# Optimization experiments

Measured on AMD Instinct MI355X. Metric: run time of the kernel, lower is better.

Reference implementation:

```python
import jax, jax.numpy as jnp
import numpy as np

L = 7
LVL = 3
B = 8
R = 16
N = 4 ** L  # 16384
P = N // 4  # number of local blocks
T = 4 * R   # ConvLocal output features


def build_permutation_indices(L, l):
    delta = 4 ** (L - l - 1)
    tmp = np.tile(np.arange(4) * delta, delta)
    tmp += np.repeat(np.arange(delta), 4)
    tmp = np.tile(tmp, 4 ** l)
    tmp += np.repeat(np.arange(4 ** l) * 4 ** (L - l), 4 ** (L - l))
    return jnp.asarray(tmp, dtype=jnp.int32)


def setup_inputs() -> dict:
    key = jax.random.key(0)
    kx, k1, k2, k3, k4 = jax.random.split(key, 5)
    scale = 1.0 / np.sqrt(T)
    x = jax.random.normal(kx, (B, 2, N, R), dtype=jnp.float32)
    # flax ConvLocal kernels: (out_spatial, kernel_size*in_features, features)
    W_rr = jax.random.normal(k1, (P, 4 * R, T), dtype=jnp.float32) * scale
    W_ri = jax.random.normal(k2, (P, 4 * R, T), dtype=jnp.float32) * scale
    W_ir = jax.random.normal(k3, (P, 4 * R, T), dtype=jnp.float32) * scale
    W_ii = jax.random.normal(k4, (P, 4 * R, T), dtype=jnp.float32) * scale
    perm_idx = build_permutation_indices(L, LVL)
    return {"x": x, "W_rr": W_rr, "W_ri": W_ri, "W_ir": W_ir,
            "W_ii": W_ii, "perm_idx": perm_idx}


def reference(x, W_rr, W_ri, W_ir, W_ii, perm_idx):
    b, _, n, r = x.shape
    p = n // 4
    # butterfly permutation gather along the spatial axis
    xp = jnp.take(x, perm_idx, axis=2)            # [B, 2, n, r]
    # group into length-4 windows; flax ConvLocal flattens (kernel, in_feat)
    xr = xp[:, 0].reshape(b, p, 4 * r)            # [B, p, 4r]
    xi = xp[:, 1].reshape(b, p, 4 * r)
    # block-diagonal (locally connected) matmuls, complex-style combine
    y_re = jnp.einsum('bpi,pio->bpo', xr, W_rr) + jnp.einsum('bpi,pio->bpo', xi, W_ri)
    y_im = jnp.einsum('bpi,pio->bpo', xr, W_ir) + jnp.einsum('bpi,pio->bpo', xi, W_ii)
    y = jnp.stack([y_re, y_im], axis=1)           # [B, 2, p, 4r]
    return y.reshape(b, 2, n, r)
```

## Files before the change

kernel.cpp:

```cpp
#include <hip/hip_runtime.h>

#define C_N 16384
#define C_R 16
#define C_P 4096
#define C_B 8

__global__ __launch_bounds__(256)
void butterfly_local_conv(const float* __restrict__ x,
                          const float* __restrict__ Wrr,
                          const float* __restrict__ Wri,
                          const float* __restrict__ Wir,
                          const float* __restrict__ Wii,
                          const int*   __restrict__ perm,
                          float* __restrict__ out)
{
    __shared__ float lds_x[4][2][C_B][64];

    const int tid    = threadIdx.x;
    const int p_base = blockIdx.x * 4;

    {
        const int pl  = tid >> 6;
        const int rem = tid & 63;
        const int c   = rem >> 5;
        const int b   = (rem >> 2) & 7;
        const int s   = rem & 3;
        const int p   = p_base + pl;
        const int n   = perm[4 * p + s];
        const float4* src = (const float4*)(x + (((size_t)(b * 2 + c)) * C_N + n) * C_R);
        float4* dst = (float4*)(&lds_x[pl][c][b][s * 16]);
        dst[0] = src[0];
        dst[1] = src[1];
        dst[2] = src[2];
        dst[3] = src[3];
    }
    __syncthreads();

    const int w = tid >> 6;
    const int o = tid & 63;
    const int p = p_base + w;

    float acc_re[C_B], acc_im[C_B];
    #pragma unroll
    for (int b = 0; b < C_B; ++b) { acc_re[b] = 0.0f; acc_im[b] = 0.0f; }

    const size_t wbase = (size_t)p * 64 * 64 + o;
    const float* __restrict__ wrr_p = Wrr + wbase;
    const float* __restrict__ wri_p = Wri + wbase;
    const float* __restrict__ wir_p = Wir + wbase;
    const float* __restrict__ wii_p = Wii + wbase;

    for (int i0 = 0; i0 < 64; i0 += 4) {
        float wrr[4], wri[4], wir[4], wii[4];
        #pragma unroll
        for (int k = 0; k < 4; ++k) {
            const int off = (i0 + k) * 64;
            wrr[k] = wrr_p[off];
            wri[k] = wri_p[off];
            wir[k] = wir_p[off];
            wii[k] = wii_p[off];
        }
        #pragma unroll
        for (int b = 0; b < C_B; ++b) {
            const float4 xr4 = *(const float4*)(&lds_x[w][0][b][i0]);
            const float4 xi4 = *(const float4*)(&lds_x[w][1][b][i0]);
            acc_re[b] = fmaf(xr4.x, wrr[0], acc_re[b]);
            acc_re[b] = fmaf(xi4.x, wri[0], acc_re[b]);
            acc_im[b] = fmaf(xr4.x, wir[0], acc_im[b]);
            acc_im[b] = fmaf(xi4.x, wii[0], acc_im[b]);

            acc_re[b] = fmaf(xr4.y, wrr[1], acc_re[b]);
            acc_re[b] = fmaf(xi4.y, wri[1], acc_re[b]);
            acc_im[b] = fmaf(xr4.y, wir[1], acc_im[b]);
            acc_im[b] = fmaf(xi4.y, wii[1], acc_im[b]);

            acc_re[b] = fmaf(xr4.z, wrr[2], acc_re[b]);
            acc_re[b] = fmaf(xi4.z, wri[2], acc_re[b]);
            acc_im[b] = fmaf(xr4.z, wir[2], acc_im[b]);
            acc_im[b] = fmaf(xi4.z, wii[2], acc_im[b]);

            acc_re[b] = fmaf(xr4.w, wrr[3], acc_re[b]);
            acc_re[b] = fmaf(xi4.w, wri[3], acc_re[b]);
            acc_im[b] = fmaf(xr4.w, wir[3], acc_im[b]);
            acc_im[b] = fmaf(xi4.w, wii[3], acc_im[b]);
        }
    }

    #pragma unroll
    for (int b = 0; b < C_B; ++b) {
        const size_t base = (size_t)p * 64 + o;
        out[((size_t)(b * 2 + 0)) * (C_N * C_R) + base] = acc_re[b];
        out[((size_t)(b * 2 + 1)) * (C_N * C_R) + base] = acc_im[b];
    }
}

extern "C" void kernel_launch(void* const* d_in, const int* in_sizes, int n_in,
                              void* d_out, int out_size, void* d_ws, size_t ws_size,
                              hipStream_t stream) {
    const float* x    = (const float*)d_in[0];
    const float* Wrr  = (const float*)d_in[1];
    const float* Wri  = (const float*)d_in[2];
    const float* Wir  = (const float*)d_in[3];
    const float* Wii  = (const float*)d_in[4];
    const int*   perm = (const int*)d_in[5];
    float* out = (float*)d_out;

    butterfly_local_conv<<<dim3(C_P / 4), dim3(256), 0, stream>>>(
        x, Wrr, Wri, Wir, Wii, perm, out);
}
```

Baseline: 268.2 us.

## Split reduction dimension across waves with one block per local patch

Each block now handles a single local block p instead of four, and its four waves each take a 16-wide slice of the 64-long input dimension (split-K). Partial sums go to shared memory and are reduced before the coalesced store. This launches four times as many blocks, each with a shorter serial dependency chain, so more loads are in flight to hide weight-streaming latency. The cost is an extra LDS round-trip and a second barrier. Launch bounds also request higher occupancy.

```diff
diff --git a/kernel.cpp b/kernel.cpp
--- a/kernel.cpp
+++ b/kernel.cpp
@@ -5,7 +5,7 @@
 #define C_P 4096
 #define C_B 8
 
-__global__ __launch_bounds__(256)
+__global__ __launch_bounds__(256, 8)
 void butterfly_local_conv(const float* __restrict__ x,
                           const float* __restrict__ Wrr,
                           const float* __restrict__ Wri,
@@ -14,47 +14,43 @@
                           const int*   __restrict__ perm,
                           float* __restrict__ out)
 {
-    __shared__ float lds_x[4][2][C_B][64];
+    __shared__ float xs[2][C_B][64];
+    __shared__ float partial[4][2][C_B][64];
 
-    const int tid    = threadIdx.x;
-    const int p_base = blockIdx.x * 4;
+    const int t = threadIdx.x;
+    const int p = blockIdx.x;
 
     {
-        const int pl  = tid >> 6;
-        const int rem = tid & 63;
-        const int c   = rem >> 5;
-        const int b   = (rem >> 2) & 7;
-        const int s   = rem & 3;
-        const int p   = p_base + pl;
-        const int n   = perm[4 * p + s];
-        const float4* src = (const float4*)(x + (((size_t)(b * 2 + c)) * C_N + n) * C_R);
-        float4* dst = (float4*)(&lds_x[pl][c][b][s * 16]);
-        dst[0] = src[0];
-        dst[1] = src[1];
-        dst[2] = src[2];
-        dst[3] = src[3];
+        const int c = t >> 7;
+        const int b = (t >> 4) & 7;
+        const int s = (t >> 2) & 3;
+        const int q = t & 3;
+        const int n = perm[4 * p + s];
+        const float4 v = ((const float4*)(x + (((size_t)(b * 2 + c)) * C_N + n) * C_R))[q];
+        ((float4*)&xs[c][b][0])[s * 4 + q] = v;
     }
     __syncthreads();
 
-    const int w = tid >> 6;
-    const int o = tid & 63;
-    const int p = p_base + w;
+    const int w = t >> 6;
+    const int o = t & 63;
+    const int ibase = w * 16;
 
     float acc_re[C_B], acc_im[C_B];
     #pragma unroll
     for (int b = 0; b < C_B; ++b) { acc_re[b] = 0.0f; acc_im[b] = 0.0f; }
 
-    const size_t wbase = (size_t)p * 64 * 64 + o;
+    const size_t wbase = (size_t)p * 64 * 64 + (size_t)ibase * 64 + o;
     const float* __restrict__ wrr_p = Wrr + wbase;
     const float* __restrict__ wri_p = Wri + wbase;
     const float* __restrict__ wir_p = Wir + wbase;
     const float* __restrict__ wii_p = Wii + wbase;
 
-    for (int i0 = 0; i0 < 64; i0 += 4) {
+    #pragma unroll
+    for (int k0 = 0; k0 < 16; k0 += 4) {
         float wrr[4], wri[4], wir[4], wii[4];
         #pragma unroll
         for (int k = 0; k < 4; ++k) {
-            const int off = (i0 + k) * 64;
+            const int off = (k0 + k) * 64;
             wrr[k] = wrr_p[off];
             wri[k] = wri_p[off];
             wir[k] = wir_p[off];
@@ -62,8 +58,8 @@
         }
         #pragma unroll
         for (int b = 0; b < C_B; ++b) {
-            const float4 xr4 = *(const float4*)(&lds_x[w][0][b][i0]);
-            const float4 xi4 = *(const float4*)(&lds_x[w][1][b][i0]);
+            const float4 xr4 = *(const float4*)(&xs[0][b][ibase + k0]);
+            const float4 xi4 = *(const float4*)(&xs[1][b][ibase + k0]);
             acc_re[b] = fmaf(xr4.x, wrr[0], acc_re[b]);
             acc_re[b] = fmaf(xi4.x, wri[0], acc_re[b]);
             acc_im[b] = fmaf(xr4.x, wir[0], acc_im[b]);
@@ -88,9 +84,19 @@
 
     #pragma unroll
     for (int b = 0; b < C_B; ++b) {
-        const size_t base = (size_t)p * 64 + o;
-        out[((size_t)(b * 2 + 0)) * (C_N * C_R) + base] = acc_re[b];
-        out[((size_t)(b * 2 + 1)) * (C_N * C_R) + base] = acc_im[b];
+        partial[w][0][b][o] = acc_re[b];
+        partial[w][1][b][o] = acc_im[b];
+    }
+    __syncthreads();
+
+    #pragma unroll
+    for (int j = 0; j < 4; ++j) {
+        const int cb = (t >> 6) * 4 + j;
+        const int c = cb >> 3;
+        const int b = cb & 7;
+        const float s = partial[0][c][b][o] + partial[1][c][b][o]
+                      + partial[2][c][b][o] + partial[3][c][b][o];
+        out[((size_t)(b * 2 + c)) * (C_N * C_R) + (size_t)p * 64 + o] = s;
     }
 }
 
@@ -105,6 +111,6 @@
     const int*   perm = (const int*)d_in[5];
     float* out = (float*)d_out;
 
-    butterfly_local_conv<<<dim3(C_P / 4), dim3(256), 0, stream>>>(
+    butterfly_local_conv<<<dim3(C_P), dim3(256), 0, stream>>>(
         x, Wrr, Wri, Wir, Wii, perm, out);
 }
```

New measurement: 268.8 us. About the same (+0.2%).
